# Performance work log

Hardware: AMD Instinct MI355X
Metric: run time of the kernel (lower is better)

The kernel has to match this reference:

```python
import jax, jax.numpy as jnp
import numpy as np

N = 65536      # nodes
E = 524288     # edges (avg degree 8)
C = 128        # in_channels == hidden_channels
L = 3          # num_layers
EPS = 1e-5     # BatchNorm eps


def setup_inputs() -> dict:
    key = jax.random.key(0)
    ks = jax.random.split(key, 12)
    inv = 1.0 / np.sqrt(C)
    return {
        "x": jax.random.normal(ks[0], (N, C), jnp.float32),
        "edge_weight": jax.random.uniform(ks[1], (E,), jnp.float32),
        "bn_gamma": 1.0 + 0.1 * jax.random.normal(ks[2], (L, C), jnp.float32),
        "bn_beta": 0.1 * jax.random.normal(ks[3], (L, C), jnp.float32),
        "W_self": inv * jax.random.normal(ks[4], (L, C, C), jnp.float32),
        "W_neigh": inv * jax.random.normal(ks[5], (L, C, C), jnp.float32),
        "bias": 0.01 * jax.random.normal(ks[6], (L, C), jnp.float32),
        "lin_w": inv * jax.random.normal(ks[7], (C,), jnp.float32),
        "lin_b": 0.01 * jax.random.normal(ks[8], (), jnp.float32),
        "src": jax.random.randint(ks[9], (E,), 0, N),
        "dst": jax.random.randint(ks[10], (E,), 0, N),
    }


def reference(x, edge_weight, bn_gamma, bn_beta, W_self, W_neigh, bias, lin_w, lin_b, src, dst):
    # log1p on edge weights (done once in the torch module per layer; identical each layer)
    ew = jnp.log1p(edge_weight)[:, None]                     # [E,1]
    # in-degree for mean aggregation (DGL fn.mean); isolated nodes -> divide by 1 (sum is 0)
    deg = jax.ops.segment_sum(jnp.ones((E,), x.dtype), dst, num_segments=N)
    deg = jnp.maximum(deg, 1.0)[:, None]                     # [N,1]

    h = x
    for l in range(L):
        # BatchNorm1d over nodes (training-mode batch stats, biased variance)
        mu = jnp.mean(h, axis=0)
        var = jnp.mean((h - mu) ** 2, axis=0)
        h = (h - mu) * jax.lax.rsqrt(var + EPS) * bn_gamma[l] + bn_beta[l]
        # SAGEConv mean aggregator: msg = h[src] * w, neigh = mean over in-edges
        msg = h[src] * ew                                    # [E,C]
        neigh = jax.ops.segment_sum(msg, dst, num_segments=N) / deg  # [N,C]
        h = jax.nn.relu(h @ W_self[l] + neigh @ W_neigh[l] + bias[l])
    return h @ lin_w + lin_b                                 # [N]
```

## Files before the change

kernel.cpp:

```cpp
#include <hip/hip_runtime.h>
#include <hip/hip_fp16.h>

#define NN 65536
#define EE 524288
#define CC 128
#define CAP 32

typedef _Float16 f16x8 __attribute__((ext_vector_type(8)));
typedef float f32x4 __attribute__((ext_vector_type(4)));


__global__ void k_init(const float* __restrict__ x, __half* __restrict__ h,
                       float* __restrict__ pstat0,
                       const int* __restrict__ src, const int* __restrict__ dst,
                       const float* __restrict__ ew,
                       int* __restrict__ cnt, unsigned int* __restrict__ buf) {
    int b = blockIdx.x, t = threadIdx.x;
    if (b < 256) {
        const float4* xv = (const float4*)x;
        __half2* o = (__half2*)h;
        float s[4] = {0, 0, 0, 0}, q[4] = {0, 0, 0, 0};
        for (int k = 0; k < 32; k++) {
            int i = b * 8192 + k * 256 + t;
            float4 v = xv[i];
            o[2 * i]     = __floats2half2_rn(v.x, v.y);
            o[2 * i + 1] = __floats2half2_rn(v.z, v.w);
            s[0] += v.x; s[1] += v.y; s[2] += v.z; s[3] += v.w;
            q[0] += v.x * v.x; q[1] += v.y * v.y; q[2] += v.z * v.z; q[3] += v.w * v.w;
        }
        __shared__ float ls[256];
        ls[t] = 0.f;
        __syncthreads();
        int c0 = (t & 31) * 4;
#pragma unroll
        for (int u = 0; u < 4; u++) {
            atomicAdd(&ls[c0 + u], s[u]);
            atomicAdd(&ls[128 + c0 + u], q[u]);
        }
        __syncthreads();
        if (t < 128) {
            atomicAdd(&pstat0[t], ls[t]);
            atomicAdd(&pstat0[128 + t], ls[128 + t]);
        }
    } else {
        int base = (b - 256) * 1024 + t;
        int dd[4], sr[4];
        float we[4];
#pragma unroll
        for (int u = 0; u < 4; u++) dd[u] = dst[base + u * 256];
#pragma unroll
        for (int u = 0; u < 4; u++) sr[u] = src[base + u * 256];
#pragma unroll
        for (int u = 0; u < 4; u++) we[u] = ew[base + u * 256];
        int pos[4];
#pragma unroll
        for (int u = 0; u < 4; u++) pos[u] = atomicAdd(&cnt[dd[u]], 1);
#pragma unroll
        for (int u = 0; u < 4; u++) {
            float w = log1pf(we[u]);
            unsigned int pk = (unsigned int)sr[u] |
                              ((unsigned int)__half_as_ushort(__float2half(w)) << 16);
            if (pos[u] < CAP) buf[dd[u] * CAP + pos[u]] = pk;
        }
    }
}


__global__ void k_aggfold(const __half2* __restrict__ h, const int* __restrict__ cnt,
                          const unsigned int* __restrict__ buf,
                          __half2* __restrict__ aggn, float* __restrict__ sod, int writeSod,
                          const float* __restrict__ pstat_l,
                          const float* __restrict__ gamma, const float* __restrict__ beta,
                          const float* __restrict__ Ws, const float* __restrict__ Wn,
                          const float* __restrict__ bias,
                          __half* __restrict__ Wcat, float* __restrict__ crow,
                          float* __restrict__ cneigh) {
    int bid = blockIdx.x;
    int tid = threadIdx.x;
    if (bid >= NN / 8) {
        int c = (bid - NN / 8) * 2 + (tid >> 7);
        int k = tid & 127;
        float mu = pstat_l[k] * (1.0f / NN);
        float var = pstat_l[128 + k] * (1.0f / NN) - mu * mu;
        float alpha = rsqrtf(var + 1e-5f) * gamma[k];
        float delta = beta[k] - mu * alpha;
        float ws = Ws[k * 128 + c];
        float wn = Wn[k * 128 + c];
        Wcat[c * 256 + k]       = __float2half(alpha * ws);
        Wcat[c * 256 + 128 + k] = __float2half(alpha * wn);
        float rs = delta * ws, rn = delta * wn;
#pragma unroll
        for (int off = 1; off < 64; off <<= 1) {
            rs += __shfl_xor(rs, off);
            rn += __shfl_xor(rn, off);
        }
        __shared__ float tmp[8];
        int wv = tid >> 6;
        if ((tid & 63) == 0) { tmp[wv * 2] = rs; tmp[wv * 2 + 1] = rn; }
        __syncthreads();
        if ((tid & 127) == 0) {
            int base = (tid >> 7) * 4;
            crow[c]   = bias[c] + tmp[base + 0] + tmp[base + 2];
            cneigh[c] = tmp[base + 1] + tmp[base + 3];
        }
        return;
    }
    int lane = tid & 63;
    int n0 = bid * 8 + (tid >> 6) * 2;
    int n1 = n0 + 1;
    int dA = cnt[n0]; if (dA > CAP) dA = CAP;
    int dB = cnt[n1]; if (dB > CAP) dB = CAP;
    unsigned int pkA = 0, pkB = 0;
    if (lane < dA) pkA = buf[n0 * CAP + lane];
    if (lane < dB) pkB = buf[n1 * CAP + lane];
    float ax[8], ay[8], bx[8], by[8];
#pragma unroll
    for (int u = 0; u < 8; u++) { ax[u] = 0.f; ay[u] = 0.f; bx[u] = 0.f; by[u] = 0.f; }
    int dmax = dA > dB ? dA : dB;
    int rounds = (dmax + 7) >> 3;
    for (int r = 0; r < rounds; r++) {
        int j = r * 8;
        unsigned int pA[8], pB[8];
        __half2 hA[8], hB[8];
#pragma unroll
        for (int u = 0; u < 8; u++) pA[u] = __shfl(pkA, j + u);
#pragma unroll
        for (int u = 0; u < 8; u++) pB[u] = __shfl(pkB, j + u);
#pragma unroll
        for (int u = 0; u < 8; u++) hA[u] = h[(pA[u] & 0xFFFF) * 64 + lane];
#pragma unroll
        for (int u = 0; u < 8; u++) hB[u] = h[(pB[u] & 0xFFFF) * 64 + lane];
#pragma unroll
        for (int u = 0; u < 8; u++) {
            float w = __half2float(__ushort_as_half((unsigned short)(pA[u] >> 16)));
            float2 v = __half22float2(hA[u]);
            ax[u] += w * v.x;
            ay[u] += w * v.y;
        }
#pragma unroll
        for (int u = 0; u < 8; u++) {
            float w = __half2float(__ushort_as_half((unsigned short)(pB[u] >> 16)));
            float2 v = __half22float2(hB[u]);
            bx[u] += w * v.x;
            by[u] += w * v.y;
        }
    }
    float axs = ((ax[0] + ax[1]) + (ax[2] + ax[3])) + ((ax[4] + ax[5]) + (ax[6] + ax[7]));
    float ays = ((ay[0] + ay[1]) + (ay[2] + ay[3])) + ((ay[4] + ay[5]) + (ay[6] + ay[7]));
    float bxs = ((bx[0] + bx[1]) + (bx[2] + bx[3])) + ((bx[4] + bx[5]) + (bx[6] + bx[7]));
    float bys = ((by[0] + by[1]) + (by[2] + by[3])) + ((by[4] + by[5]) + (by[6] + by[7]));
    float invA = 1.0f / (float)(dA > 1 ? dA : 1);
    float invB = 1.0f / (float)(dB > 1 ? dB : 1);
    aggn[n0 * 64 + lane] = __floats2half2_rn(axs * invA, ays * invA);
    aggn[n1 * 64 + lane] = __floats2half2_rn(bxs * invB, bys * invB);
    if (writeSod) {
        float wA = __half2float(__ushort_as_half((unsigned short)(pkA >> 16)));
        float wB = __half2float(__ushort_as_half((unsigned short)(pkB >> 16)));
#pragma unroll
        for (int off = 1; off < 64; off <<= 1) {
            wA += __shfl_xor(wA, off);
            wB += __shfl_xor(wB, off);
        }
        if (lane == 0) { sod[n0] = wA * invA; sod[n1] = wB * invB; }
    }
}

__launch_bounds__(256, 2)
__global__ void k_gemm(const __half* hA, const __half* __restrict__ aggn,
                       const __half* __restrict__ Wcat,
                       const float* __restrict__ crow, const float* __restrict__ cneigh,
                       const float* __restrict__ sod,
                       const float* __restrict__ lin_w, const float* __restrict__ lin_b,
                       __half* hout, float* __restrict__ outv, int mode,
                       float* __restrict__ pstatN) {
    __shared__ __half Bl[128 * 136];
    int tid = threadIdx.x;
    int lane = tid & 63;
    int wvid = tid >> 6;
    int l15 = lane & 15, quad = lane >> 4;
    int i0 = blockIdx.x * 128;

    f32x4 acc0[8], acc1[8];
    f32x4 zero = {0.f, 0.f, 0.f, 0.f};
#pragma unroll
    for (int t = 0; t < 8; t++) { acc0[t] = zero; acc1[t] = zero; }

#pragma unroll
    for (int chunk = 0; chunk < 2; chunk++) {
        const __half* Asrc = chunk ? aggn : hA;
        f16x8 af0[4], af1[4];
#pragma unroll
        for (int s = 0; s < 4; s++) {
            int kof = s * 32 + quad * 8;
            af0[s] = *(const f16x8*)&Asrc[(i0 + wvid * 32 + l15) * 128 + kof];
            af1[s] = *(const f16x8*)&Asrc[(i0 + wvid * 32 + 16 + l15) * 128 + kof];
        }
        __syncthreads();
#pragma unroll
        for (int it = 0; it < 8; it++) {
            int m = tid * 8 + it * 2048;
            int c = m >> 7, kl = m & 127;
            *(f16x8*)&Bl[c * 136 + kl] = *(const f16x8*)&Wcat[c * 256 + chunk * 128 + kl];
        }
        __syncthreads();
#pragma unroll
        for (int s = 0; s < 4; s++) {
#pragma unroll
            for (int tn = 0; tn < 8; tn++) {
                f16x8 bf = *(const f16x8*)&Bl[(tn * 16 + l15) * 136 + s * 32 + quad * 8];
                acc0[tn] = __builtin_amdgcn_mfma_f32_16x16x32_f16(af0[s], bf, acc0[tn], 0, 0, 0);
                acc1[tn] = __builtin_amdgcn_mfma_f32_16x16x32_f16(af1[s], bf, acc1[tn], 0, 0, 0);
            }
        }
    }

    float cr[8], cn[8];
#pragma unroll
    for (int tn = 0; tn < 8; tn++) {
        cr[tn] = crow[tn * 16 + l15];
        cn[tn] = cneigh[tn * 16 + l15];
    }
    int rwbase = i0 + wvid * 32 + quad * 4;

    if (mode == 0) {
        float cs[8], cq[8];
#pragma unroll
        for (int tn = 0; tn < 8; tn++) { cs[tn] = 0.f; cq[tn] = 0.f; }
#pragma unroll
        for (int tm = 0; tm < 2; tm++) {
#pragma unroll
            for (int r = 0; r < 4; r++) {
                int row = rwbase + tm * 16 + r;
                float sdv = sod[row];
#pragma unroll
                for (int tn = 0; tn < 8; tn++) {
                    float v = (tm ? acc1[tn][r] : acc0[tn][r]) + cr[tn] + sdv * cn[tn];
                    v = fmaxf(v, 0.f);
                    hout[row * 128 + tn * 16 + l15] = __float2half(v);
                    cs[tn] += v;
                    cq[tn] += v * v;
                }
            }
        }
#pragma unroll
        for (int tn = 0; tn < 8; tn++) {
            cs[tn] += __shfl_xor(cs[tn], 16); cs[tn] += __shfl_xor(cs[tn], 32);
            cq[tn] += __shfl_xor(cq[tn], 16); cq[tn] += __shfl_xor(cq[tn], 32);
        }
        __syncthreads();
        float* st = (float*)Bl;
        st[tid] = 0.f;
        __syncthreads();
        if (lane < 16) {
#pragma unroll
            for (int tn = 0; tn < 8; tn++) {
                atomicAdd(&st[tn * 16 + l15], cs[tn]);
                atomicAdd(&st[128 + tn * 16 + l15], cq[tn]);
            }
        }
        __syncthreads();
        if (tid < 128) {
            atomicAdd(&pstatN[tid], st[tid]);
            atomicAdd(&pstatN[128 + tid], st[128 + tid]);
        }
    } else {
        float lw[8];
#pragma unroll
        for (int tn = 0; tn < 8; tn++) lw[tn] = lin_w[tn * 16 + l15];
        float lb = lin_b[0];
#pragma unroll
        for (int tm = 0; tm < 2; tm++) {
#pragma unroll
            for (int r = 0; r < 4; r++) {
                int row = rwbase + tm * 16 + r;
                float sdv = sod[row];
                float p = 0.f;
#pragma unroll
                for (int tn = 0; tn < 8; tn++) {
                    float v = (tm ? acc1[tn][r] : acc0[tn][r]) + cr[tn] + sdv * cn[tn];
                    v = fmaxf(v, 0.f);
                    p += v * lw[tn];
                }
                p += __shfl_xor(p, 1);
                p += __shfl_xor(p, 2);
                p += __shfl_xor(p, 4);
                p += __shfl_xor(p, 8);
                if (l15 == 0) outv[row] = p + lb;
            }
        }
    }
}


extern "C" void kernel_launch(void* const* d_in, const int* in_sizes, int n_in,
                              void* d_out, int out_size, void* d_ws, size_t ws_size,
                              hipStream_t stream) {
    (void)in_sizes; (void)n_in; (void)out_size; (void)ws_size;
    const float* x     = (const float*)d_in[0];
    const float* ew    = (const float*)d_in[1];
    const float* gamma = (const float*)d_in[2];
    const float* beta  = (const float*)d_in[3];
    const float* Ws    = (const float*)d_in[4];
    const float* Wn    = (const float*)d_in[5];
    const float* bias  = (const float*)d_in[6];
    const float* lin_w = (const float*)d_in[7];
    const float* lin_b = (const float*)d_in[8];
    const int*   srcI  = (const int*)d_in[9];
    const int*   dstI  = (const int*)d_in[10];
    float* out = (float*)d_out;

    char* p = (char*)d_ws;
    __half* h    = (__half*)p; p += (size_t)NN * CC * 2;
    __half* aggn = (__half*)p; p += (size_t)NN * CC * 2;
    __half* Wcat = (__half*)p; p += 256 * 128 * 2;
    float* crow   = (float*)p; p += 512;
    float* cneigh = (float*)p; p += 512;
    float* sod    = (float*)p; p += (size_t)NN * 4;
    unsigned int* buf = (unsigned int*)p; p += (size_t)NN * CAP * 4;
    int*   cnt    = (int*)p;   p += (size_t)NN * 4;
    float* pstat  = (float*)p; p += 3 * 256 * 4;

    hipMemsetAsync(cnt, 0, (size_t)NN * 4 + 3 * 256 * 4, stream);

    k_init<<<dim3(256 + EE / 1024), dim3(256), 0, stream>>>(x, h, pstat, srcI, dstI, ew, cnt, buf);

    for (int l = 0; l < 3; l++) {
        k_aggfold<<<dim3(NN / 8 + 64), dim3(256), 0, stream>>>(
            (const __half2*)h, cnt, buf, (__half2*)aggn, sod, (l == 0) ? 1 : 0,
            pstat + l * 256, gamma + l * CC, beta + l * CC,
            Ws + (size_t)l * CC * CC, Wn + (size_t)l * CC * CC, bias + l * CC,
            Wcat, crow, cneigh);
        int mode = (l == 2) ? 1 : 0;
        float* pstatN = (mode == 0) ? (pstat + (l + 1) * 256) : pstat;
        k_gemm<<<dim3(NN / 128), dim3(256), 0, stream>>>(h, aggn, Wcat, crow, cneigh, sod,
                                                         lin_w, lin_b, h, out, mode, pstatN);
    }
}
```

Baseline: 272.4 us.

## Fuse neighbor aggregation into GEMM kernel via LDS tile, ping-pong h buffers

```diff
diff --git a/kernel.cpp b/kernel.cpp
--- a/kernel.cpp
+++ b/kernel.cpp
@@ -66,119 +66,142 @@
 }
 
 
-__global__ void k_aggfold(const __half2* __restrict__ h, const int* __restrict__ cnt,
-                          const unsigned int* __restrict__ buf,
-                          __half2* __restrict__ aggn, float* __restrict__ sod, int writeSod,
-                          const float* __restrict__ pstat_l,
-                          const float* __restrict__ gamma, const float* __restrict__ beta,
-                          const float* __restrict__ Ws, const float* __restrict__ Wn,
-                          const float* __restrict__ bias,
-                          __half* __restrict__ Wcat, float* __restrict__ crow,
-                          float* __restrict__ cneigh) {
+__global__ void k_fold(const float* __restrict__ pstat_l,
+                       const float* __restrict__ gamma, const float* __restrict__ beta,
+                       const float* __restrict__ Ws, const float* __restrict__ Wn,
+                       const float* __restrict__ bias,
+                       __half* __restrict__ Wcat, float* __restrict__ crow,
+                       float* __restrict__ cneigh) {
     int bid = blockIdx.x;
     int tid = threadIdx.x;
-    if (bid >= NN / 8) {
-        int c = (bid - NN / 8) * 2 + (tid >> 7);
-        int k = tid & 127;
-        float mu = pstat_l[k] * (1.0f / NN);
-        float var = pstat_l[128 + k] * (1.0f / NN) - mu * mu;
-        float alpha = rsqrtf(var + 1e-5f) * gamma[k];
-        float delta = beta[k] - mu * alpha;
-        float ws = Ws[k * 128 + c];
-        float wn = Wn[k * 128 + c];
-        Wcat[c * 256 + k]       = __float2half(alpha * ws);
-        Wcat[c * 256 + 128 + k] = __float2half(alpha * wn);
-        float rs = delta * ws, rn = delta * wn;
-#pragma unroll
-        for (int off = 1; off < 64; off <<= 1) {
-            rs += __shfl_xor(rs, off);
-            rn += __shfl_xor(rn, off);
-        }
-        __shared__ float tmp[8];
-        int wv = tid >> 6;
-        if ((tid & 63) == 0) { tmp[wv * 2] = rs; tmp[wv * 2 + 1] = rn; }
-        __syncthreads();
-        if ((tid & 127) == 0) {
-            int base = (tid >> 7) * 4;
-            crow[c]   = bias[c] + tmp[base + 0] + tmp[base + 2];
-            cneigh[c] = tmp[base + 1] + tmp[base + 3];
-        }
-        return;
-    }
-    int lane = tid & 63;
-    int n0 = bid * 8 + (tid >> 6) * 2;
-    int n1 = n0 + 1;
-    int dA = cnt[n0]; if (dA > CAP) dA = CAP;
-    int dB = cnt[n1]; if (dB > CAP) dB = CAP;
-    unsigned int pkA = 0, pkB = 0;
-    if (lane < dA) pkA = buf[n0 * CAP + lane];
-    if (lane < dB) pkB = buf[n1 * CAP + lane];
-    float ax[8], ay[8], bx[8], by[8];
-#pragma unroll
-    for (int u = 0; u < 8; u++) { ax[u] = 0.f; ay[u] = 0.f; bx[u] = 0.f; by[u] = 0.f; }
-    int dmax = dA > dB ? dA : dB;
-    int rounds = (dmax + 7) >> 3;
-    for (int r = 0; r < rounds; r++) {
-        int j = r * 8;
-        unsigned int pA[8], pB[8];
-        __half2 hA[8], hB[8];
-#pragma unroll
-        for (int u = 0; u < 8; u++) pA[u] = __shfl(pkA, j + u);
-#pragma unroll
-        for (int u = 0; u < 8; u++) pB[u] = __shfl(pkB, j + u);
-#pragma unroll
-        for (int u = 0; u < 8; u++) hA[u] = h[(pA[u] & 0xFFFF) * 64 + lane];
-#pragma unroll
-        for (int u = 0; u < 8; u++) hB[u] = h[(pB[u] & 0xFFFF) * 64 + lane];
-#pragma unroll
-        for (int u = 0; u < 8; u++) {
-            float w = __half2float(__ushort_as_half((unsigned short)(pA[u] >> 16)));
-            float2 v = __half22float2(hA[u]);
-            ax[u] += w * v.x;
-            ay[u] += w * v.y;
-        }
-#pragma unroll
-        for (int u = 0; u < 8; u++) {
-            float w = __half2float(__ushort_as_half((unsigned short)(pB[u] >> 16)));
-            float2 v = __half22float2(hB[u]);
-            bx[u] += w * v.x;
-            by[u] += w * v.y;
-        }
-    }
-    float axs = ((ax[0] + ax[1]) + (ax[2] + ax[3])) + ((ax[4] + ax[5]) + (ax[6] + ax[7]));
-    float ays = ((ay[0] + ay[1]) + (ay[2] + ay[3])) + ((ay[4] + ay[5]) + (ay[6] + ay[7]));
-    float bxs = ((bx[0] + bx[1]) + (bx[2] + bx[3])) + ((bx[4] + bx[5]) + (bx[6] + bx[7]));
-    float bys = ((by[0] + by[1]) + (by[2] + by[3])) + ((by[4] + by[5]) + (by[6] + by[7]));
-    float invA = 1.0f / (float)(dA > 1 ? dA : 1);
-    float invB = 1.0f / (float)(dB > 1 ? dB : 1);
-    aggn[n0 * 64 + lane] = __floats2half2_rn(axs * invA, ays * invA);
-    aggn[n1 * 64 + lane] = __floats2half2_rn(bxs * invB, bys * invB);
-    if (writeSod) {
-        float wA = __half2float(__ushort_as_half((unsigned short)(pkA >> 16)));
-        float wB = __half2float(__ushort_as_half((unsigned short)(pkB >> 16)));
-#pragma unroll
-        for (int off = 1; off < 64; off <<= 1) {
-            wA += __shfl_xor(wA, off);
-            wB += __shfl_xor(wB, off);
-        }
-        if (lane == 0) { sod[n0] = wA * invA; sod[n1] = wB * invB; }
+    int c = bid * 2 + (tid >> 7);
+    int k = tid & 127;
+    float mu = pstat_l[k] * (1.0f / NN);
+    float var = pstat_l[128 + k] * (1.0f / NN) - mu * mu;
+    float alpha = rsqrtf(var + 1e-5f) * gamma[k];
+    float delta = beta[k] - mu * alpha;
+    float ws = Ws[k * 128 + c];
+    float wn = Wn[k * 128 + c];
+    Wcat[c * 256 + k]       = __float2half(alpha * ws);
+    Wcat[c * 256 + 128 + k] = __float2half(alpha * wn);
+    float rs = delta * ws, rn = delta * wn;
+#pragma unroll
+    for (int off = 1; off < 64; off <<= 1) {
+        rs += __shfl_xor(rs, off);
+        rn += __shfl_xor(rn, off);
+    }
+    __shared__ float tmp[8];
+    int wv = tid >> 6;
+    if ((tid & 63) == 0) { tmp[wv * 2] = rs; tmp[wv * 2 + 1] = rn; }
+    __syncthreads();
+    if ((tid & 127) == 0) {
+        int base = (tid >> 7) * 4;
+        crow[c]   = bias[c] + tmp[base + 0] + tmp[base + 2];
+        cneigh[c] = tmp[base + 1] + tmp[base + 3];
     }
 }
 
 __launch_bounds__(256, 2)
-__global__ void k_gemm(const __half* hA, const __half* __restrict__ aggn,
-                       const __half* __restrict__ Wcat,
-                       const float* __restrict__ crow, const float* __restrict__ cneigh,
-                       const float* __restrict__ sod,
-                       const float* __restrict__ lin_w, const float* __restrict__ lin_b,
-                       __half* hout, float* __restrict__ outv, int mode,
-                       float* __restrict__ pstatN) {
+__global__ void k_layer(const __half* __restrict__ hin,
+                        const int* __restrict__ cnt,
+                        const unsigned int* __restrict__ buf,
+                        const __half* __restrict__ Wcat,
+                        const float* __restrict__ crow, const float* __restrict__ cneigh,
+                        float* __restrict__ sod, int writeSod,
+                        const float* __restrict__ lin_w, const float* __restrict__ lin_b,
+                        __half* __restrict__ hout, float* __restrict__ outv, int mode,
+                        float* __restrict__ pstatN) {
     __shared__ __half Bl[128 * 136];
+    __shared__ __half aggT[128 * 136];
+    __shared__ float sodT[128];
     int tid = threadIdx.x;
     int lane = tid & 63;
     int wvid = tid >> 6;
     int l15 = lane & 15, quad = lane >> 4;
     int i0 = blockIdx.x * 128;
+    int rbase = i0 + wvid * 32;
+
+    f16x8 as0[4], as1[4];
+#pragma unroll
+    for (int s = 0; s < 4; s++) {
+        int kof = s * 32 + quad * 8;
+        as0[s] = *(const f16x8*)&hin[(rbase + l15) * 128 + kof];
+        as1[s] = *(const f16x8*)&hin[(rbase + 16 + l15) * 128 + kof];
+    }
+
+    const __half2* h2 = (const __half2*)hin;
+    int dv = 0;
+    if (lane < 32) { dv = cnt[rbase + lane]; if (dv > CAP) dv = CAP; }
+    int dA = __shfl(dv, 0), dB = __shfl(dv, 1);
+    unsigned int pkA = 0, pkB = 0;
+    if (lane < dA) pkA = buf[(rbase + 0) * CAP + lane];
+    if (lane < dB) pkB = buf[(rbase + 1) * CAP + lane];
+
+    for (int pair = 0; pair < 16; ++pair) {
+        int ndA = 0, ndB = 0;
+        unsigned int npA = 0, npB = 0;
+        if (pair < 15) {
+            ndA = __shfl(dv, 2 * pair + 2);
+            ndB = __shfl(dv, 2 * pair + 3);
+            if (lane < ndA) npA = buf[(rbase + 2 * pair + 2) * CAP + lane];
+            if (lane < ndB) npB = buf[(rbase + 2 * pair + 3) * CAP + lane];
+        }
+        float ax[8], ay[8], bx[8], by[8];
+#pragma unroll
+        for (int u = 0; u < 8; u++) { ax[u] = 0.f; ay[u] = 0.f; bx[u] = 0.f; by[u] = 0.f; }
+        int dmax = dA > dB ? dA : dB;
+        int rounds = (dmax + 7) >> 3;
+        for (int r = 0; r < rounds; r++) {
+            int j = r * 8;
+            unsigned int pA[8], pB[8];
+            __half2 hA[8], hB[8];
+#pragma unroll
+            for (int u = 0; u < 8; u++) pA[u] = __shfl(pkA, j + u);
+#pragma unroll
+            for (int u = 0; u < 8; u++) pB[u] = __shfl(pkB, j + u);
+#pragma unroll
+            for (int u = 0; u < 8; u++) hA[u] = h2[(pA[u] & 0xFFFF) * 64 + lane];
+#pragma unroll
+            for (int u = 0; u < 8; u++) hB[u] = h2[(pB[u] & 0xFFFF) * 64 + lane];
+#pragma unroll
+            for (int u = 0; u < 8; u++) {
+                float w = __half2float(__ushort_as_half((unsigned short)(pA[u] >> 16)));
+                float2 v = __half22float2(hA[u]);
+                ax[u] += w * v.x;
+                ay[u] += w * v.y;
+            }
+#pragma unroll
+            for (int u = 0; u < 8; u++) {
+                float w = __half2float(__ushort_as_half((unsigned short)(pB[u] >> 16)));
+                float2 v = __half22float2(hB[u]);
+                bx[u] += w * v.x;
+                by[u] += w * v.y;
+            }
+        }
+        float axs = ((ax[0] + ax[1]) + (ax[2] + ax[3])) + ((ax[4] + ax[5]) + (ax[6] + ax[7]));
+        float ays = ((ay[0] + ay[1]) + (ay[2] + ay[3])) + ((ay[4] + ay[5]) + (ay[6] + ay[7]));
+        float bxs = ((bx[0] + bx[1]) + (bx[2] + bx[3])) + ((bx[4] + bx[5]) + (bx[6] + bx[7]));
+        float bys = ((by[0] + by[1]) + (by[2] + by[3])) + ((by[4] + by[5]) + (by[6] + by[7]));
+        float invA = 1.0f / (float)(dA > 1 ? dA : 1);
+        float invB = 1.0f / (float)(dB > 1 ? dB : 1);
+        int rloc = wvid * 32 + 2 * pair;
+        *(__half2*)&aggT[rloc * 136 + 2 * lane]       = __floats2half2_rn(axs * invA, ays * invA);
+        *(__half2*)&aggT[(rloc + 1) * 136 + 2 * lane] = __floats2half2_rn(bxs * invB, bys * invB);
+        if (writeSod) {
+            float wA = __half2float(__ushort_as_half((unsigned short)(pkA >> 16)));
+            float wB = __half2float(__ushort_as_half((unsigned short)(pkB >> 16)));
+#pragma unroll
+            for (int off = 1; off < 64; off <<= 1) {
+                wA += __shfl_xor(wA, off);
+                wB += __shfl_xor(wB, off);
+            }
+            if (lane == 0) {
+                sodT[rloc] = wA * invA;     sod[i0 + rloc] = wA * invA;
+                sodT[rloc + 1] = wB * invB; sod[i0 + rloc + 1] = wB * invB;
+            }
+        }
+        dA = ndA; dB = ndB; pkA = npA; pkB = npB;
+    }
 
     f32x4 acc0[8], acc1[8];
     f32x4 zero = {0.f, 0.f, 0.f, 0.f};
@@ -186,31 +209,40 @@
     for (int t = 0; t < 8; t++) { acc0[t] = zero; acc1[t] = zero; }
 
 #pragma unroll
-    for (int chunk = 0; chunk < 2; chunk++) {
-        const __half* Asrc = chunk ? aggn : hA;
-        f16x8 af0[4], af1[4];
-#pragma unroll
-        for (int s = 0; s < 4; s++) {
-            int kof = s * 32 + quad * 8;
-            af0[s] = *(const f16x8*)&Asrc[(i0 + wvid * 32 + l15) * 128 + kof];
-            af1[s] = *(const f16x8*)&Asrc[(i0 + wvid * 32 + 16 + l15) * 128 + kof];
-        }
-        __syncthreads();
-#pragma unroll
-        for (int it = 0; it < 8; it++) {
-            int m = tid * 8 + it * 2048;
-            int c = m >> 7, kl = m & 127;
-            *(f16x8*)&Bl[c * 136 + kl] = *(const f16x8*)&Wcat[c * 256 + chunk * 128 + kl];
-        }
-        __syncthreads();
-#pragma unroll
-        for (int s = 0; s < 4; s++) {
-#pragma unroll
-            for (int tn = 0; tn < 8; tn++) {
-                f16x8 bf = *(const f16x8*)&Bl[(tn * 16 + l15) * 136 + s * 32 + quad * 8];
-                acc0[tn] = __builtin_amdgcn_mfma_f32_16x16x32_f16(af0[s], bf, acc0[tn], 0, 0, 0);
-                acc1[tn] = __builtin_amdgcn_mfma_f32_16x16x32_f16(af1[s], bf, acc1[tn], 0, 0, 0);
-            }
+    for (int it = 0; it < 8; it++) {
+        int m = tid * 8 + it * 2048;
+        int c = m >> 7, kl = m & 127;
+        *(f16x8*)&Bl[c * 136 + kl] = *(const f16x8*)&Wcat[c * 256 + kl];
+    }
+    __syncthreads();
+#pragma unroll
+    for (int s = 0; s < 4; s++) {
+        int kof = s * 32 + quad * 8;
+#pragma unroll
+        for (int tn = 0; tn < 8; tn++) {
+            f16x8 bf = *(const f16x8*)&Bl[(tn * 16 + l15) * 136 + kof];
+            acc0[tn] = __builtin_amdgcn_mfma_f32_16x16x32_f16(as0[s], bf, acc0[tn], 0, 0, 0);
+            acc1[tn] = __builtin_amdgcn_mfma_f32_16x16x32_f16(as1[s], bf, acc1[tn], 0, 0, 0);
+        }
+    }
+    __syncthreads();
+#pragma unroll
+    for (int it = 0; it < 8; it++) {
+        int m = tid * 8 + it * 2048;
+        int c = m >> 7, kl = m & 127;
+        *(f16x8*)&Bl[c * 136 + kl] = *(const f16x8*)&Wcat[c * 256 + 128 + kl];
+    }
+    __syncthreads();
+#pragma unroll
+    for (int s = 0; s < 4; s++) {
+        int kof = s * 32 + quad * 8;
+        f16x8 an0 = *(const f16x8*)&aggT[(wvid * 32 + l15) * 136 + kof];
+        f16x8 an1 = *(const f16x8*)&aggT[(wvid * 32 + 16 + l15) * 136 + kof];
+#pragma unroll
+        for (int tn = 0; tn < 8; tn++) {
+            f16x8 bf = *(const f16x8*)&Bl[(tn * 16 + l15) * 136 + kof];
+            acc0[tn] = __builtin_amdgcn_mfma_f32_16x16x32_f16(an0, bf, acc0[tn], 0, 0, 0);
+            acc1[tn] = __builtin_amdgcn_mfma_f32_16x16x32_f16(an1, bf, acc1[tn], 0, 0, 0);
         }
     }
 
@@ -231,7 +263,7 @@
 #pragma unroll
             for (int r = 0; r < 4; r++) {
                 int row = rwbase + tm * 16 + r;
-                float sdv = sod[row];
+                float sdv = writeSod ? sodT[row - i0] : sod[row];
 #pragma unroll
                 for (int tn = 0; tn < 8; tn++) {
                     float v = (tm ? acc1[tn][r] : acc0[tn][r]) + cr[tn] + sdv * cn[tn];
@@ -310,8 +342,8 @@
     float* out = (float*)d_out;
 
     char* p = (char*)d_ws;
-    __half* h    = (__half*)p; p += (size_t)NN * CC * 2;
-    __half* aggn = (__half*)p; p += (size_t)NN * CC * 2;
+    __half* ha   = (__half*)p; p += (size_t)NN * CC * 2;
+    __half* hb   = (__half*)p; p += (size_t)NN * CC * 2;
     __half* Wcat = (__half*)p; p += 256 * 128 * 2;
     float* crow   = (float*)p; p += 512;
     float* cneigh = (float*)p; p += 512;
@@ -322,17 +354,20 @@
 
     hipMemsetAsync(cnt, 0, (size_t)NN * 4 + 3 * 256 * 4, stream);
 
-    k_init<<<dim3(256 + EE / 1024), dim3(256), 0, stream>>>(x, h, pstat, srcI, dstI, ew, cnt, buf);
-
+    k_init<<<dim3(256 + EE / 1024), dim3(256), 0, stream>>>(x, ha, pstat, srcI, dstI, ew, cnt, buf);
+
+    const __half* hin = ha;
+    __half* hout = hb;
     for (int l = 0; l < 3; l++) {
-        k_aggfold<<<dim3(NN / 8 + 64), dim3(256), 0, stream>>>(
-            (const __half2*)h, cnt, buf, (__half2*)aggn, sod, (l == 0) ? 1 : 0,
+        k_fold<<<dim3(64), dim3(256), 0, stream>>>(
             pstat + l * 256, gamma + l * CC, beta + l * CC,
             Ws + (size_t)l * CC * CC, Wn + (size_t)l * CC * CC, bias + l * CC,
             Wcat, crow, cneigh);
         int mode = (l == 2) ? 1 : 0;
         float* pstatN = (mode == 0) ? (pstat + (l + 1) * 256) : pstat;
-        k_gemm<<<dim3(NN / 128), dim3(256), 0, stream>>>(h, aggn, Wcat, crow, cneigh, sod,
-                                                         lin_w, lin_b, h, out, mode, pstatN);
+        k_layer<<<dim3(NN / 128), dim3(256), 0, stream>>>(
+            hin, cnt, buf, Wcat, crow, cneigh, sod, (l == 0) ? 1 : 0,
+            lin_w, lin_b, hout, out, mode, pstatN);
+        const __half* t = hin; hin = hout; hout = (__half*)t;
     }
 }
```

New measurement: 278.3 us. +2.2%, slower.
